# Performance work log

Measured on AMD Instinct MI355X. Metric: run time of the kernel, lower is better.

## Reference

```python
import jax, jax.numpy as jnp
import numpy as np

# static config (matches init_kwargs)
NH, NKV, E, K = 16, 4, 8, 2
CAP_FACTOR = 1.25
LN_EPS = 1e-5


def _layer_norm(x, w, b):
    mu = jnp.mean(x, axis=-1, keepdims=True)
    var = jnp.mean(jnp.square(x - mu), axis=-1, keepdims=True)
    return (x - mu) * jax.lax.rsqrt(var + LN_EPS) * w + b


def setup_inputs() -> dict:
    key = jax.random.key(0)
    ks = jax.random.split(key, 6)
    S, B, H, F = 2048, 1, 1024, 2048
    HD = H // NH
    qkv_out = NKV * ((NH // NKV) + 2) * HD  # 1536
    f32 = jnp.float32
    return {
        "hidden_states": jax.random.normal(ks[0], (S, B, H), f32),
        "ln1_weight": jnp.ones((H,), f32),
        "ln1_bias": jnp.zeros((H,), f32),
        "ln2_weight": jnp.ones((H,), f32),
        "ln2_bias": jnp.zeros((H,), f32),
        "qkv_weight": jax.random.normal(ks[1], (qkv_out, H), f32) * 0.02,
        "proj_weight": jax.random.normal(ks[2], (H, H), f32) * 0.02,
        "router_weight": jax.random.normal(ks[3], (H, E), f32) * 0.02,
        "moe_w1": jax.random.normal(ks[4], (E, H, F), f32) * 0.02,
        "moe_w2": jax.random.normal(ks[5], (F and E, F, H), f32)[:E] * 0.02 if False else jax.random.normal(ks[5], (E, F, H), f32) * 0.02,
    }


def reference(hidden_states, ln1_weight, ln1_bias, ln2_weight, ln2_bias,
              qkv_weight, proj_weight, router_weight, moe_w1, moe_w2):
    S, B, H = hidden_states.shape
    HD = H // NH
    q_per_kv = NH // NKV
    # ---- attention block (cp_size=1: all-to-alls are identity) ----
    ln1 = _layer_norm(hidden_states, ln1_weight, ln1_bias)
    qkv = jnp.einsum('sbh,oh->sbo', ln1, qkv_weight)
    qkv = qkv.reshape(S, B, NKV, (q_per_kv + 2) * HD)
    q = qkv[..., : q_per_kv * HD].reshape(S, B, NH, HD)
    k = qkv[..., q_per_kv * HD:(q_per_kv + 1) * HD]          # [S,B,NKV,HD]
    v = qkv[..., (q_per_kv + 1) * HD:]                        # [S,B,NKV,HD]
    qb = jnp.transpose(q, (1, 2, 0, 3)).reshape(B, NKV, q_per_kv, S, HD)
    kb = jnp.transpose(k, (1, 2, 0, 3))                       # [B,NKV,S,HD]
    vb = jnp.transpose(v, (1, 2, 0, 3))
    scale = 1.0 / np.sqrt(HD).astype(np.float32)
    scores = jnp.einsum('bgqsd,bgtd->bgqst', qb, kb) * scale  # [B,NKV,qpk,S,S]
    causal = jnp.tril(jnp.ones((S, S), bool))
    scores = jnp.where(causal, scores, jnp.finfo(scores.dtype).min)
    attn = jax.nn.softmax(scores, axis=-1)
    ao = jnp.einsum('bgqst,bgtd->bgqsd', attn, vb)
    ao = ao.reshape(B, NH, S, HD)
    ao = jnp.transpose(ao, (2, 0, 1, 3)).reshape(S, B, H)
    proj = jnp.einsum('sbh,oh->sbo', ao, proj_weight)
    h1 = hidden_states + proj
    # ---- MoE block (ep_size=1: uniform all-to-all is identity) ----
    ln2 = _layer_norm(h1, ln2_weight, ln2_bias)
    x = ln2.reshape(-1, H)                                    # [N,H]
    N = x.shape[0]
    logits = x @ router_weight                                # linear(x, router_weight.t())
    probs = jax.nn.softmax(logits, axis=-1)
    top_p, top_i = jax.lax.top_k(probs, K)
    top_p = top_p / jnp.sum(top_p, axis=-1, keepdims=True)
    exp_idx = top_i.reshape(-1)                               # [N*K]
    exp_p = top_p.reshape(-1)
    # stable sort by expert id, capacity-padded dispatch
    order = jnp.argsort(exp_idx, stable=True)
    sorted_exp = exp_idx[order]
    counts = jnp.bincount(exp_idx, length=E)
    offsets = jnp.concatenate([jnp.zeros((1,), counts.dtype), jnp.cumsum(counts)[:-1]])
    within = jnp.arange(N * K) - offsets[sorted_exp]
    cap = int(np.ceil(N * K / E * CAP_FACTOR))
    T = E * cap
    valid = within < cap
    dst = jnp.where(valid, sorted_exp * cap + within, T)      # T = out-of-bounds -> dropped
    padded_tokens = jnp.zeros((T, H), x.dtype).at[dst].set(x[order // K], mode='drop')
    padded_probs = jnp.zeros((T,), exp_p.dtype).at[dst].set(exp_p[order], mode='drop')
    padded_tid = jnp.zeros((T,), jnp.int32).at[dst].set((order // K).astype(jnp.int32), mode='drop')
    # grouped expert GEMMs: [E,cap,H] x [E,H,F] -> gelu -> [E,cap,H]
    xt = padded_tokens.reshape(E, cap, H)
    fc1 = jax.nn.gelu(jnp.einsum('ech,ehf->ecf', xt, moe_w1))
    fc2 = jnp.einsum('ecf,efh->ech', fc1, moe_w2).reshape(T, H)
    weighted = fc2 * padded_probs[:, None]                    # pad slots have prob 0
    moe_out = jnp.zeros((N, H), hidden_states.dtype).at[padded_tid].add(weighted)
    return h1 + moe_out.reshape(S, B, H)
```

## Files before the change

kernel.cpp:

```cpp
#include <hip/hip_runtime.h>
#include <hip/hip_bf16.h>
#include <stdint.h>

#define S_LEN 2048
#define HDIM  1024
#define NHEAD 16
#define NKVH  4
#define HEADD 64
#define QKV_O 1536
#define NEXP  8
#define TOPK  2
#define CAP   640
#define TCAP  (NEXP*CAP)
#define FDIM  2048
#define LOG2E 1.44269504088896f
#define NCHUNK 40

typedef __bf16 bf16x8 __attribute__((ext_vector_type(8)));
typedef float  f32x4  __attribute__((ext_vector_type(4)));
typedef unsigned int u32;
typedef u32 u32x4 __attribute__((ext_vector_type(4)));
typedef u32 u32x2 __attribute__((ext_vector_type(2)));
typedef unsigned short u16;
typedef u16 u16x8 __attribute__((ext_vector_type(8)));

__device__ __forceinline__ void gload16(const __bf16* g, __bf16* l) {
    __builtin_amdgcn_global_load_lds(
        (const __attribute__((address_space(1))) u32*)g,
        (__attribute__((address_space(3))) u32*)l, 16, 0, 0);
}

__device__ __constant__ const signed char c_strip[NCHUNK] =
    {0,1,2,3, 4,4, 5,5, 6,6, 7,7, 8,8,8, 9,9,9, 10,10,10, 11,11,11,
     12,12,12,12, 13,13,13,13, 14,14,14,14, 15,15,15,15};
__device__ __constant__ const signed char c_chunk[NCHUNK] =
    {0,0,0,0, 0,1, 0,1, 0,1, 0,1, 0,1,2, 0,1,2, 0,1,2, 0,1,2,
     0,1,2,3, 0,1,2,3, 0,1,2,3, 0,1,2,3};
__device__ __constant__ const signed char c_cbase[16] = {0,1,2,3,4,6,8,10,12,15,18,21,24,28,32,36};
__device__ __constant__ const signed char c_nch[16]   = {1,1,1,1,2,2,2,2,3,3,3,3,4,4,4,4};

__global__ __launch_bounds__(256)
void prep_kernel(const float* __restrict__ hidden, const float* __restrict__ ln1w,
                 const float* __restrict__ ln1bb, const float* __restrict__ qkvW,
                 const float* __restrict__ projW, __bf16* __restrict__ ln1o,
                 __bf16* __restrict__ qkvWb, __bf16* __restrict__ projWb) {
    const int b = blockIdx.x, tid = threadIdx.x;
    if (b < S_LEN) {
        __shared__ float red[256];
        const float* x = hidden + (size_t)b * HDIM;
        float s = 0.f;
        for (int i = tid; i < HDIM; i += 256) s += x[i];
        red[tid] = s; __syncthreads();
        for (int st = 128; st > 0; st >>= 1) { if (tid < st) red[tid] += red[tid+st]; __syncthreads(); }
        float mu = red[0] / HDIM; __syncthreads();
        float v = 0.f;
        for (int i = tid; i < HDIM; i += 256) { float d = x[i]-mu; v += d*d; }
        red[tid] = v; __syncthreads();
        for (int st = 128; st > 0; st >>= 1) { if (tid < st) red[tid] += red[tid+st]; __syncthreads(); }
        float rstd = rsqrtf(red[0]/HDIM + 1e-5f);
        for (int i = tid; i < HDIM; i += 256)
            ln1o[(size_t)b*HDIM + i] = (__bf16)((x[i]-mu)*rstd*ln1w[i] + ln1bb[i]);
        return;
    }
    const float* src; __bf16* dst; int i;
    if (b < S_LEN + 768) { src = qkvW; dst = qkvWb; i = (b - S_LEN)*256 + tid; }
    else                 { src = projW; dst = projWb; i = (b - S_LEN - 768)*256 + tid; }
    const float4* s = (const float4*)src + (size_t)i*2;
    float4 a = s[0], b4 = s[1];
    __bf16 tmp[8] = {(__bf16)a.x,(__bf16)a.y,(__bf16)a.z,(__bf16)a.w,
                     (__bf16)b4.x,(__bf16)b4.y,(__bf16)b4.z,(__bf16)b4.w};
    *(u32x4*)(dst + (size_t)i*8) = *(u32x4*)tmp;
}

__global__ __launch_bounds__(256)
void transp2_kernel(const float* __restrict__ w1, const float* __restrict__ w2,
                    __bf16* __restrict__ w1t, __bf16* __restrict__ w2t) {
    __shared__ float t[32][33];
    const int b = blockIdx.x;
    const float* src; __bf16* dst; int K, N, n0, k0, e;
    if (b < 16384) {
        e = b >> 11; int rem = b & 2047;
        K = HDIM; N = FDIM; n0 = (rem & 63) * 32; k0 = (rem >> 6) * 32;
        src = w1 + (size_t)e*K*N; dst = w1t + (size_t)e*K*N;
    } else {
        int bb = b - 16384; e = bb >> 11; int rem = bb & 2047;
        K = FDIM; N = HDIM; n0 = (rem & 31) * 32; k0 = (rem >> 5) * 32;
        src = w2 + (size_t)e*K*N; dst = w2t + (size_t)e*K*N;
    }
    int tx = threadIdx.x & 31, ty = threadIdx.x >> 5;
    #pragma unroll
    for (int i = 0; i < 32; i += 8)
        t[ty+i][tx] = src[(size_t)(k0+ty+i)*N + n0 + tx];
    __syncthreads();
    #pragma unroll
    for (int i = 0; i < 32; i += 8)
        dst[(size_t)(n0+ty+i)*K + k0 + tx] = (__bf16)t[tx][ty+i];
}

template<int EPI>
__global__ __launch_bounds__(256)
void gemm_bf16_kernel(const __bf16* __restrict__ A, const __bf16* __restrict__ Bt,
                      const float* __restrict__ R, void* __restrict__ Cout,
                      int N, int K, long sA, long sB, long sC) {
    __shared__ __bf16 As[128*64];
    __shared__ __bf16 Bs[128*64];
    const int e = blockIdx.z;
    A  += (size_t)e * sA;
    Bt += (size_t)e * sB;
    const int m0 = blockIdx.y*128, n0 = blockIdx.x*128;
    const int tid = threadIdx.x;
    const int lane = tid & 63, w = tid >> 6;
    const int lr = lane & 15, lg = lane >> 4;
    const int wr = w >> 1, wc = w & 1;
    const int srow8 = lane >> 3, sg = lane & 7;
    f32x4 acc[4][4] = {};
    for (int k0 = 0; k0 < K; k0 += 64) {
        __syncthreads();
        #pragma unroll
        for (int i = 0; i < 4; ++i) {
            int row = 32*w + 8*i + srow8;
            int src_g = sg ^ (row & 7);
            gload16(A  + (size_t)(m0+row)*K + k0 + src_g*8,
                    (__bf16*)((char*)As + (32*w + 8*i)*128));
            gload16(Bt + (size_t)(n0+row)*K + k0 + src_g*8,
                    (__bf16*)((char*)Bs + (32*w + 8*i)*128));
        }
        __syncthreads();
        #pragma unroll
        for (int ks = 0; ks < 2; ++ks) {
            bf16x8 af[4], bfr[4];
            #pragma unroll
            for (int mi = 0; mi < 4; ++mi) {
                int row = wr*64 + mi*16 + lr;
                af[mi] = *(const bf16x8*)((const char*)As + ((row*128 + (lg+4*ks)*16) ^ ((row&7)<<4)));
            }
            #pragma unroll
            for (int ni = 0; ni < 4; ++ni) {
                int row = wc*64 + ni*16 + lr;
                bfr[ni] = *(const bf16x8*)((const char*)Bs + ((row*128 + (lg+4*ks)*16) ^ ((row&7)<<4)));
            }
            #pragma unroll
            for (int mi = 0; mi < 4; ++mi)
                #pragma unroll
                for (int ni = 0; ni < 4; ++ni)
                    acc[mi][ni] = __builtin_amdgcn_mfma_f32_16x16x32_bf16(af[mi], bfr[ni], acc[mi][ni], 0,0,0);
        }
    }
    #pragma unroll
    for (int mi = 0; mi < 4; ++mi) {
        #pragma unroll
        for (int ni = 0; ni < 4; ++ni) {
            #pragma unroll
            for (int r = 0; r < 4; ++r) {
                int row = m0 + wr*64 + mi*16 + lg*4 + r;
                int col = n0 + wc*64 + ni*16 + lr;
                float v = acc[mi][ni][r];
                if (EPI == 1) v += R[(size_t)row*N + col];
                if (EPI == 2) {
                    float t = 0.7978845608028654f * (v + 0.044715f*v*v*v);
                    v = 0.5f * v * (1.f + tanhf(t));
                }
                if (EPI == 2 || EPI == 3)
                    ((__bf16*)Cout)[(size_t)e*sC + (size_t)row*N + col] = (__bf16)v;
                else
                    ((float*)Cout)[(size_t)e*sC + (size_t)row*N + col] = v;
            }
        }
    }
}

__global__ __launch_bounds__(512)
void attn_part_kernel(const __bf16* __restrict__ qkv, float* __restrict__ partO,
                      float* __restrict__ partML) {
    const int cx = blockIdx.x;
    const int h  = blockIdx.y;
    const int hg = h >> 2, qi = h & 3;
    const int qb = c_strip[cx];
    const int t0 = 4 * c_chunk[cx];
    const int t1 = min(qb + 1, t0 + 4);
    const int q0 = qb * 128;
    const int tid  = threadIdx.x;
    const int w    = tid >> 6;
    const int lane = tid & 63;
    const int lr   = lane & 15;
    const int lg   = lane >> 4;

    __shared__ __attribute__((aligned(16))) __bf16 Kls[128*64];
    __shared__ __attribute__((aligned(16))) __bf16 Vls[64*128];
    __shared__ __attribute__((aligned(16))) __bf16 Pls[8][16*128];

    const int krow = tid >> 2, kc = (tid & 3) * 2;
    const int va = tid & 63,  dg  = tid >> 6;
    u32x4 kreg[2]; u16x8 vreg[2];

    const __bf16* kbase = qkv + hg*384 + 256;
    const __bf16* vbase = qkv + hg*384 + 320;

#define ISSUE(T) do { \
        const __bf16* kp = kbase + (size_t)((T)*128 + krow)*QKV_O + kc*8; \
        kreg[0] = *(const u32x4*)(kp); \
        kreg[1] = *(const u32x4*)(kp + 8); \
        const __bf16* vp = vbase + (size_t)((T)*128 + 2*va)*QKV_O + dg*8; \
        vreg[0] = *(const u16x8*)(vp); \
        vreg[1] = *(const u16x8*)(vp + QKV_O); \
    } while(0)

#define COMMIT() do { \
        char* Kb = (char*)Kls; \
        *(u32x4*)(Kb + ((krow*128 + (kc+0)*16) ^ ((krow&7)<<4))) = kreg[0]; \
        *(u32x4*)(Kb + ((krow*128 + (kc+1)*16) ^ ((krow&7)<<4))) = kreg[1]; \
        char* Vb = (char*)Vls; \
        _Pragma("unroll") \
        for (int j = 0; j < 8; ++j) { \
            int d = dg*8 + j; \
            u32 u = ((u32)vreg[1][j] << 16) | vreg[0][j]; \
            *(u32*)(Vb + ((d*256 + va*4) ^ ((d&7)<<4))) = u; \
        } \
    } while(0)

    const int qrow = q0 + w*16 + lr;
    const __bf16* qp = qkv + (size_t)qrow*QKV_O + hg*384 + qi*64;
    bf16x8 qfrag[2];
    #pragma unroll
    for (int ks = 0; ks < 2; ++ks) {
        bf16x8 qr = *(const bf16x8*)(qp + ks*32 + lg*8);
        #pragma unroll
        for (int j = 0; j < 8; ++j) qfrag[ks][j] = (__bf16)((float)qr[j] * 0.125f);
    }
    bf16x8 ones;
    #pragma unroll
    for (int j = 0; j < 8; ++j) ones[j] = (__bf16)1.0f;

    f32x4 oacc[4] = {};
    f32x4 lcol = {};
    float mrow[4] = {-INFINITY,-INFINITY,-INFINITY,-INFINITY};

    ISSUE(t0);
    for (int t = t0; t < t1; ++t) {
        __syncthreads();
        COMMIT();
        if (t+1 < t1) ISSUE(t+1);
        __syncthreads();

        f32x4 sacc[8] = {};
        const char* Kb = (const char*)Kls;
        #pragma unroll
        for (int f = 0; f < 8; ++f) {
            int row = lr + 16*f;
            int swz = (row & 7) << 4;
            #pragma unroll
            for (int ks = 0; ks < 2; ++ks) {
                bf16x8 kf = *(const bf16x8*)(Kb + ((row*128 + (lg*8+32*ks)*2) ^ swz));
                sacc[f] = __builtin_amdgcn_mfma_f32_16x16x32_bf16(qfrag[ks], kf, sacc[f], 0,0,0);
            }
        }
        if (t == qb) {
            #pragma unroll
            for (int f = 0; f < 8; ++f)
                #pragma unroll
                for (int r = 0; r < 4; ++r)
                    if (lr + 16*f > 16*w + 4*lg + r) sacc[f][r] = -INFINITY;
        }
        float tm[4];
        #pragma unroll
        for (int r = 0; r < 4; ++r) {
            float a = fmaxf(fmaxf(sacc[0][r], sacc[1][r]), fmaxf(sacc[2][r], sacc[3][r]));
            float b2 = fmaxf(fmaxf(sacc[4][r], sacc[5][r]), fmaxf(sacc[6][r], sacc[7][r]));
            tm[r] = fmaxf(a, b2);
        }
        #pragma unroll
        for (int msk = 1; msk < 16; msk <<= 1)
            #pragma unroll
            for (int r = 0; r < 4; ++r) tm[r] = fmaxf(tm[r], __shfl_xor(tm[r], msk, 64));
        float corr[4];
        #pragma unroll
        for (int r = 0; r < 4; ++r) {
            float mn = fmaxf(mrow[r], tm[r]);
            corr[r] = exp2f((mrow[r]-mn)*LOG2E);
            mrow[r] = mn;
        }
        #pragma unroll
        for (int f = 0; f < 8; ++f)
            #pragma unroll
            for (int r = 0; r < 4; ++r)
                sacc[f][r] = exp2f((sacc[f][r]-mrow[r])*LOG2E);
        #pragma unroll
        for (int ct = 0; ct < 4; ++ct)
            #pragma unroll
            for (int r = 0; r < 4; ++r) oacc[ct][r] *= corr[r];
        #pragma unroll
        for (int r = 0; r < 4; ++r) lcol[r] *= corr[r];
        char* Pw = (char*)&Pls[w][0];
        #pragma unroll
        for (int f = 0; f < 8; ++f)
            #pragma unroll
            for (int r = 0; r < 4; ++r) {
                int row = 4*lg + r, col = lr + 16*f;
                *(__bf16*)(Pw + ((row*256 + col*2) ^ ((row&7)<<4))) = (__bf16)sacc[f][r];
            }
        const char* Vb = (const char*)Vls;
        bf16x8 pa[4];
        #pragma unroll
        for (int ks = 0; ks < 4; ++ks)
            pa[ks] = *(const bf16x8*)(Pw + ((lr*256 + (lg*8+32*ks)*2) ^ ((lr&7)<<4)));
        #pragma unroll
        for (int ks = 0; ks < 4; ++ks)
            lcol = __builtin_amdgcn_mfma_f32_16x16x32_bf16(pa[ks], ones, lcol, 0,0,0);
        #pragma unroll
        for (int ct = 0; ct < 4; ++ct) {
            int row = lr + 16*ct;
            int swz = (row & 7) << 4;
            #pragma unroll
            for (int ks = 0; ks < 4; ++ks) {
                bf16x8 vf = *(const bf16x8*)(Vb + ((row*256 + (lg*8+32*ks)*2) ^ swz));
                oacc[ct] = __builtin_amdgcn_mfma_f32_16x16x32_bf16(pa[ks], vf, oacc[ct], 0,0,0);
            }
        }
    }
    const int p = h*NCHUNK + cx;
    float* po = partO + (size_t)p * (128*64);
    #pragma unroll
    for (int ct = 0; ct < 4; ++ct)
        #pragma unroll
        for (int r = 0; r < 4; ++r)
            po[(16*w + 4*lg + r)*64 + 16*ct + lr] = oacc[ct][r];
    if (lr == 0) {
        float* pm = partML + (size_t)p * 256;
        #pragma unroll
        for (int r = 0; r < 4; ++r) {
            pm[(16*w + 4*lg + r)*2    ] = mrow[r];
            pm[(16*w + 4*lg + r)*2 + 1] = lcol[r];
        }
    }
#undef ISSUE
#undef COMMIT
}

__global__ __launch_bounds__(256)
void attn_combine_kernel(const float* __restrict__ partO, const float* __restrict__ partML,
                         __bf16* __restrict__ ao) {
    const int rb = blockIdx.x, h = blockIdx.y;
    const int row0 = rb*8;
    const int qb = row0 >> 7;
    const int nc = c_nch[qb], cb = c_cbase[qb];
    const int tid = threadIdx.x;
    const int rl = tid >> 5, d2 = (tid & 31) * 2;
    const int grow = row0 + rl;
    const int srow = grow & 127;
    const int pbase = h*NCHUNK + cb;
    float mv[4], lv[4];
    float M = -INFINITY;
    for (int c = 0; c < nc; ++c) {
        const float* pm = partML + (size_t)(pbase+c)*256 + srow*2;
        mv[c] = pm[0]; lv[c] = pm[1];
        M = fmaxf(M, mv[c]);
    }
    float L = 0.f, a0 = 0.f, a1 = 0.f;
    for (int c = 0; c < nc; ++c) {
        float wc = exp2f((mv[c]-M)*LOG2E);
        L += wc * lv[c];
        const float* po = partO + (size_t)(pbase+c)*(128*64) + srow*64 + d2;
        a0 += wc * po[0];
        a1 += wc * po[1];
    }
    float inv = 1.f / L;
    __bf16 o2[2] = {(__bf16)(a0*inv), (__bf16)(a1*inv)};
    *(u32*)(ao + (size_t)grow*HDIM + h*64 + d2) = *(u32*)o2;
}

__global__ __launch_bounds__(256)
void ln2_router_kernel(const float* __restrict__ h1, const float* __restrict__ w,
                       const float* __restrict__ b, const float* __restrict__ rw,
                       __bf16* __restrict__ x2b, int* __restrict__ expi,
                       float* __restrict__ expp) {
    const int t = blockIdx.x, tid = threadIdx.x;
    __shared__ float red[256];
    __shared__ float red8[256][8];
    const float* x = h1 + (size_t)t*HDIM;
    float s = 0.f;
    for (int i = tid; i < HDIM; i += 256) s += x[i];
    red[tid] = s; __syncthreads();
    for (int st = 128; st > 0; st >>= 1) { if (tid < st) red[tid] += red[tid+st]; __syncthreads(); }
    float mu = red[0] / HDIM; __syncthreads();
    float v = 0.f;
    for (int i = tid; i < HDIM; i += 256) { float d = x[i]-mu; v += d*d; }
    red[tid] = v; __syncthreads();
    for (int st = 128; st > 0; st >>= 1) { if (tid < st) red[tid] += red[tid+st]; __syncthreads(); }
    float rstd = rsqrtf(red[0]/HDIM + 1e-5f);
    float part[8] = {};
    for (int i = tid; i < HDIM; i += 256) {
        float o = (x[i]-mu)*rstd*w[i] + b[i];
        x2b[(size_t)t*HDIM + i] = (__bf16)o;
        const float* wp = rw + (size_t)i*NEXP;
        #pragma unroll
        for (int e2 = 0; e2 < 8; ++e2) part[e2] += o * wp[e2];
    }
    #pragma unroll
    for (int e2 = 0; e2 < 8; ++e2) red8[tid][e2] = part[e2];
    __syncthreads();
    for (int st = 128; st > 0; st >>= 1) {
        if (tid < st)
            #pragma unroll
            for (int e2 = 0; e2 < 8; ++e2) red8[tid][e2] += red8[tid+st][e2];
        __syncthreads();
    }
    if (tid == 0) {
        float lg[8];
        #pragma unroll
        for (int e2 = 0; e2 < 8; ++e2) lg[e2] = red8[0][e2];
        int i0 = 0;
        for (int e2 = 1; e2 < 8; ++e2) if (lg[e2] > lg[i0]) i0 = e2;
        int i1 = -1;
        for (int e2 = 0; e2 < 8; ++e2) { if (e2 == i0) continue; if (i1 < 0 || lg[e2] > lg[i1]) i1 = e2; }
        float p1 = __expf(lg[i1] - lg[i0]);
        float inv = 1.f / (1.f + p1);
        expi[t*2]   = i0; expi[t*2+1] = i1;
        expp[t*2]   = inv; expp[t*2+1] = p1 * inv;
    }
}

__global__ __launch_bounds__(256)
void dst_fast_kernel(const int* __restrict__ expi, int* __restrict__ dst) {
    __shared__ int hist[256][9];
    const int tid = threadIdx.x;
    int ev[16];
    #pragma unroll
    for (int i = 0; i < 16; i += 4)
        *(int4*)(ev+i) = *(const int4*)(expi + tid*16 + i);
    int cnt[8] = {};
    #pragma unroll
    for (int i = 0; i < 16; ++i)
        #pragma unroll
        for (int e = 0; e < 8; ++e) cnt[e] += (ev[i] == e);
    #pragma unroll
    for (int e = 0; e < 8; ++e) hist[tid][e] = cnt[e];
    __syncthreads();
    const int w = tid >> 6, lane = tid & 63;
    #pragma unroll
    for (int rep = 0; rep < 2; ++rep) {
        int e = w + rep*4;
        int h0 = hist[4*lane+0][e], h1 = hist[4*lane+1][e],
            h2 = hist[4*lane+2][e], h3 = hist[4*lane+3][e];
        int s = h0+h1+h2+h3, inc = s;
        #pragma unroll
        for (int off = 1; off < 64; off <<= 1) {
            int v = __shfl_up(inc, off, 64);
            if (lane >= off) inc += v;
        }
        int excl = inc - s;
        hist[4*lane+0][e] = excl;
        hist[4*lane+1][e] = excl + h0;
        hist[4*lane+2][e] = excl + h0 + h1;
        hist[4*lane+3][e] = excl + h0 + h1 + h2;
    }
    __syncthreads();
    int run[8];
    #pragma unroll
    for (int e = 0; e < 8; ++e) run[e] = hist[tid][e];
    int out[16];
    #pragma unroll
    for (int i = 0; i < 16; ++i) {
        int e = ev[i], within = 0;
        #pragma unroll
        for (int e2 = 0; e2 < 8; ++e2)
            if (e == e2) { within = run[e2]; run[e2]++; }
        out[i] = (within < CAP) ? (e*CAP + within) : -1;
    }
    #pragma unroll
    for (int i = 0; i < 16; i += 4)
        *(int4*)(dst + tid*16 + i) = *(const int4*)(out+i);
}

__global__ void scatter_kernel(const __bf16* __restrict__ x2b, const int* __restrict__ dst,
                               __bf16* __restrict__ xt) {
    int s = blockIdx.x;
    int d = dst[s];
    if (d < 0) return;
    int t = s >> 1;
    int i = threadIdx.x;
    u32x2 v = *(const u32x2*)(x2b + (size_t)t*HDIM + i*4);
    *(u32x2*)(xt + (size_t)d*HDIM + i*4) = v;
}

__global__ void combine_kernel(const float* __restrict__ h1, const float* __restrict__ fc2,
                               const int* __restrict__ dst, const float* __restrict__ expp,
                               float* __restrict__ out) {
    int t = blockIdx.x;
    int d0 = dst[t*2], d1 = dst[t*2+1];
    float p0 = expp[t*2], p1 = expp[t*2+1];
    for (int i = threadIdx.x; i < HDIM; i += 256) {
        float v = h1[(size_t)t*HDIM + i];
        if (d0 >= 0) v += p0 * fc2[(size_t)d0*HDIM + i];
        if (d1 >= 0) v += p1 * fc2[(size_t)d1*HDIM + i];
        out[(size_t)t*HDIM + i] = v;
    }
}

extern "C" void kernel_launch(void* const* d_in, const int* in_sizes, int n_in,
                              void* d_out, int out_size, void* d_ws, size_t ws_size,
                              hipStream_t stream) {
    const float* hidden = (const float*)d_in[0];
    const float* ln1w   = (const float*)d_in[1];
    const float* ln1b_  = (const float*)d_in[2];
    const float* ln2w   = (const float*)d_in[3];
    const float* ln2b_  = (const float*)d_in[4];
    const float* qkvW   = (const float*)d_in[5];
    const float* projW  = (const float*)d_in[6];
    const float* routW  = (const float*)d_in[7];
    const float* w1     = (const float*)d_in[8];
    const float* w2     = (const float*)d_in[9];
    float* out = (float*)d_out;

    char* base = (char*)d_ws;
    __bf16* w1t    = (__bf16*)(base);
    __bf16* w2t    = (__bf16*)(base + 33554432);
    __bf16* ln1b   = (__bf16*)(base + 0);
    __bf16* qkvWb  = (__bf16*)(base + 4194304);
    __bf16* qkvb   = (__bf16*)(base + 7340032);
    __bf16* aob    = (__bf16*)(base + 13631488);
    __bf16* projWb = (__bf16*)(base + 17825792);
    char* B0 = base + 67108864;
    float*  h1   = (float*)(B0);
    __bf16* xtb  = (__bf16*)(B0 + 8388608);
    __bf16* fc1b = (__bf16*)(B0 + 18874368);
    float*  fc2  = (float*)(B0 + 39845888);
    __bf16* x2b  = (__bf16*)fc2;
    int*    expi = (int*)(B0 + 60817408);
    int*    dsts = (int*)(B0 + 60833792);
    float*  expp = (float*)(B0 + 60850176);
    float*  partML = (float*)xtb;
    float*  partO  = (float*)fc1b;

    prep_kernel<<<S_LEN + 768 + 512, 256, 0, stream>>>(
        hidden, ln1w, ln1b_, qkvW, projW, ln1b, qkvWb, projWb);
    gemm_bf16_kernel<3><<<dim3(QKV_O/128, S_LEN/128, 1), 256, 0, stream>>>(
        ln1b, qkvWb, nullptr, qkvb, QKV_O, HDIM, 0, 0, 0);
    attn_part_kernel<<<dim3(NCHUNK, NHEAD), 512, 0, stream>>>(qkvb, partO, partML);
    attn_combine_kernel<<<dim3(S_LEN/8, NHEAD), 256, 0, stream>>>(partO, partML, aob);
    gemm_bf16_kernel<1><<<dim3(HDIM/128, S_LEN/128, 1), 256, 0, stream>>>(
        aob, projWb, hidden, h1, HDIM, HDIM, 0, 0, 0);
    ln2_router_kernel<<<S_LEN, 256, 0, stream>>>(h1, ln2w, ln2b_, routW, x2b, expi, expp);
    dst_fast_kernel<<<1, 256, 0, stream>>>(expi, dsts);
    scatter_kernel<<<S_LEN*TOPK, 256, 0, stream>>>(x2b, dsts, xtb);
    transp2_kernel<<<32768, 256, 0, stream>>>(w1, w2, w1t, w2t);
    gemm_bf16_kernel<2><<<dim3(FDIM/128, CAP/128, NEXP), 256, 0, stream>>>(
        xtb, w1t, nullptr, fc1b, FDIM, HDIM,
        (long)CAP*HDIM, (long)FDIM*HDIM, (long)CAP*FDIM);
    gemm_bf16_kernel<0><<<dim3(HDIM/128, CAP/128, NEXP), 256, 0, stream>>>(
        fc1b, w2t, nullptr, fc2, HDIM, FDIM,
        (long)CAP*FDIM, (long)FDIM*HDIM, (long)CAP*HDIM);
    combine_kernel<<<S_LEN, 256, 0, stream>>>(h1, fc2, dsts, expp, out);
}
```

Measured before the change: 255.7 us.

## Vectorize weight transpose, cache rows in LayerNorm, vectorize MoE combine

The expert-weight transpose kernel now uses 64x64 tiles, reading rows with float4 loads and writing 16-byte bf16 stores, so it launches a quarter as many blocks. Both LayerNorm kernels keep each thread's four elements in registers instead of reloading them from global memory for every pass. The MoE combine kernel switches to float4 loads and stores. The prep_kernel parameter order is also swapped to match the swapped call arguments, which leaves behaviour unchanged. The transpose of the 128 MB of fp32 expert weights is probably the main cost these changes target, and the larger LDS tile may lower occupancy.

```diff
diff --git a/kernel.cpp b/kernel.cpp
--- a/kernel.cpp
+++ b/kernel.cpp
@@ -43,23 +43,29 @@
 void prep_kernel(const float* __restrict__ hidden, const float* __restrict__ ln1w,
                  const float* __restrict__ ln1bb, const float* __restrict__ qkvW,
                  const float* __restrict__ projW, __bf16* __restrict__ ln1o,
-                 __bf16* __restrict__ qkvWb, __bf16* __restrict__ projWb) {
+                 __bf16* __restrict__ projWb, __bf16* __restrict__ qkvWb) {
     const int b = blockIdx.x, tid = threadIdx.x;
     if (b < S_LEN) {
         __shared__ float red[256];
         const float* x = hidden + (size_t)b * HDIM;
-        float s = 0.f;
-        for (int i = tid; i < HDIM; i += 256) s += x[i];
+        float xr[4];
+        #pragma unroll
+        for (int j = 0; j < 4; ++j) xr[j] = x[tid + 256*j];
+        float s = xr[0] + xr[1] + xr[2] + xr[3];
         red[tid] = s; __syncthreads();
         for (int st = 128; st > 0; st >>= 1) { if (tid < st) red[tid] += red[tid+st]; __syncthreads(); }
         float mu = red[0] / HDIM; __syncthreads();
         float v = 0.f;
-        for (int i = tid; i < HDIM; i += 256) { float d = x[i]-mu; v += d*d; }
+        #pragma unroll
+        for (int j = 0; j < 4; ++j) { float d = xr[j]-mu; v += d*d; }
         red[tid] = v; __syncthreads();
         for (int st = 128; st > 0; st >>= 1) { if (tid < st) red[tid] += red[tid+st]; __syncthreads(); }
         float rstd = rsqrtf(red[0]/HDIM + 1e-5f);
-        for (int i = tid; i < HDIM; i += 256)
-            ln1o[(size_t)b*HDIM + i] = (__bf16)((x[i]-mu)*rstd*ln1w[i] + ln1bb[i]);
+        #pragma unroll
+        for (int j = 0; j < 4; ++j) {
+            int i = tid + 256*j;
+            ln1o[(size_t)b*HDIM + i] = (__bf16)((xr[j]-mu)*rstd*ln1w[i] + ln1bb[i]);
+        }
         return;
     }
     const float* src; __bf16* dst; int i;
@@ -75,26 +81,36 @@
 __global__ __launch_bounds__(256)
 void transp2_kernel(const float* __restrict__ w1, const float* __restrict__ w2,
                     __bf16* __restrict__ w1t, __bf16* __restrict__ w2t) {
-    __shared__ float t[32][33];
+    __shared__ float t[64][65];
     const int b = blockIdx.x;
-    const float* src; __bf16* dst; int K, N, n0, k0, e;
-    if (b < 16384) {
-        e = b >> 11; int rem = b & 2047;
-        K = HDIM; N = FDIM; n0 = (rem & 63) * 32; k0 = (rem >> 6) * 32;
+    const float* src; __bf16* dst; int K, N, n0, k0;
+    if (b < 4096) {
+        int e = b >> 9, rem = b & 511;
+        K = HDIM; N = FDIM; n0 = (rem & 31) * 64; k0 = (rem >> 5) * 64;
         src = w1 + (size_t)e*K*N; dst = w1t + (size_t)e*K*N;
     } else {
-        int bb = b - 16384; e = bb >> 11; int rem = bb & 2047;
-        K = FDIM; N = HDIM; n0 = (rem & 31) * 32; k0 = (rem >> 5) * 32;
+        int bb = b - 4096; int e = bb >> 9, rem = bb & 511;
+        K = FDIM; N = HDIM; n0 = (rem & 15) * 64; k0 = (rem >> 4) * 64;
         src = w2 + (size_t)e*K*N; dst = w2t + (size_t)e*K*N;
     }
-    int tx = threadIdx.x & 31, ty = threadIdx.x >> 5;
-    #pragma unroll
-    for (int i = 0; i < 32; i += 8)
-        t[ty+i][tx] = src[(size_t)(k0+ty+i)*N + n0 + tx];
+    const int tid = threadIdx.x;
+    const int r = tid >> 4, c4 = (tid & 15) * 4;
+    #pragma unroll
+    for (int i = 0; i < 4; ++i) {
+        float4 v = *(const float4*)(src + (size_t)(k0 + r + 16*i)*N + n0 + c4);
+        t[r+16*i][c4+0] = v.x; t[r+16*i][c4+1] = v.y;
+        t[r+16*i][c4+2] = v.z; t[r+16*i][c4+3] = v.w;
+    }
     __syncthreads();
-    #pragma unroll
-    for (int i = 0; i < 32; i += 8)
-        dst[(size_t)(n0+ty+i)*K + k0 + tx] = (__bf16)t[tx][ty+i];
+    const int rn = tid >> 3, kc = (tid & 7) * 8;
+    #pragma unroll
+    for (int i = 0; i < 2; ++i) {
+        int n = rn + 32*i;
+        __bf16 tmp[8];
+        #pragma unroll
+        for (int j = 0; j < 8; ++j) tmp[j] = (__bf16)t[kc+j][n];
+        *(u32x4*)(dst + (size_t)(n0+n)*K + k0 + kc) = *(u32x4*)tmp;
+    }
 }
 
 template<int EPI>
@@ -377,19 +393,24 @@
     __shared__ float red[256];
     __shared__ float red8[256][8];
     const float* x = h1 + (size_t)t*HDIM;
-    float s = 0.f;
-    for (int i = tid; i < HDIM; i += 256) s += x[i];
+    float xr[4];
+    #pragma unroll
+    for (int j = 0; j < 4; ++j) xr[j] = x[tid + 256*j];
+    float s = xr[0] + xr[1] + xr[2] + xr[3];
     red[tid] = s; __syncthreads();
     for (int st = 128; st > 0; st >>= 1) { if (tid < st) red[tid] += red[tid+st]; __syncthreads(); }
     float mu = red[0] / HDIM; __syncthreads();
     float v = 0.f;
-    for (int i = tid; i < HDIM; i += 256) { float d = x[i]-mu; v += d*d; }
+    #pragma unroll
+    for (int j = 0; j < 4; ++j) { float d = xr[j]-mu; v += d*d; }
     red[tid] = v; __syncthreads();
     for (int st = 128; st > 0; st >>= 1) { if (tid < st) red[tid] += red[tid+st]; __syncthreads(); }
     float rstd = rsqrtf(red[0]/HDIM + 1e-5f);
     float part[8] = {};
-    for (int i = tid; i < HDIM; i += 256) {
-        float o = (x[i]-mu)*rstd*w[i] + b[i];
+    #pragma unroll
+    for (int j = 0; j < 4; ++j) {
+        int i = tid + 256*j;
+        float o = (xr[j]-mu)*rstd*w[i] + b[i];
         x2b[(size_t)t*HDIM + i] = (__bf16)o;
         const float* wp = rw + (size_t)i*NEXP;
         #pragma unroll
@@ -488,12 +509,17 @@
     int t = blockIdx.x;
     int d0 = dst[t*2], d1 = dst[t*2+1];
     float p0 = expp[t*2], p1 = expp[t*2+1];
-    for (int i = threadIdx.x; i < HDIM; i += 256) {
-        float v = h1[(size_t)t*HDIM + i];
-        if (d0 >= 0) v += p0 * fc2[(size_t)d0*HDIM + i];
-        if (d1 >= 0) v += p1 * fc2[(size_t)d1*HDIM + i];
-        out[(size_t)t*HDIM + i] = v;
-    }
+    int i = threadIdx.x * 4;
+    float4 v = *(const float4*)(h1 + (size_t)t*HDIM + i);
+    if (d0 >= 0) {
+        float4 f = *(const float4*)(fc2 + (size_t)d0*HDIM + i);
+        v.x += p0*f.x; v.y += p0*f.y; v.z += p0*f.z; v.w += p0*f.w;
+    }
+    if (d1 >= 0) {
+        float4 f = *(const float4*)(fc2 + (size_t)d1*HDIM + i);
+        v.x += p1*f.x; v.y += p1*f.y; v.z += p1*f.z; v.w += p1*f.w;
+    }
+    *(float4*)(out + (size_t)t*HDIM + i) = v;
 }
 
 extern "C" void kernel_launch(void* const* d_in, const int* in_sizes, int n_in,
@@ -532,7 +558,7 @@
     float*  partO  = (float*)fc1b;
 
     prep_kernel<<<S_LEN + 768 + 512, 256, 0, stream>>>(
-        hidden, ln1w, ln1b_, qkvW, projW, ln1b, qkvWb, projWb);
+        hidden, ln1w, ln1b_, qkvW, projW, ln1b, projWb, qkvWb);
     gemm_bf16_kernel<3><<<dim3(QKV_O/128, S_LEN/128, 1), 256, 0, stream>>>(
         ln1b, qkvWb, nullptr, qkvb, QKV_O, HDIM, 0, 0, 0);
     attn_part_kernel<<<dim3(NCHUNK, NHEAD), 512, 0, stream>>>(qkvb, partO, partML);
@@ -542,7 +568,7 @@
     ln2_router_kernel<<<S_LEN, 256, 0, stream>>>(h1, ln2w, ln2b_, routW, x2b, expi, expp);
     dst_fast_kernel<<<1, 256, 0, stream>>>(expi, dsts);
     scatter_kernel<<<S_LEN*TOPK, 256, 0, stream>>>(x2b, dsts, xtb);
-    transp2_kernel<<<32768, 256, 0, stream>>>(w1, w2, w1t, w2t);
+    transp2_kernel<<<8192, 256, 0, stream>>>(w1, w2, w1t, w2t);
     gemm_bf16_kernel<2><<<dim3(FDIM/128, CAP/128, NEXP), 256, 0, stream>>>(
         xtb, w1t, nullptr, fc1b, FDIM, HDIM,
         (long)CAP*HDIM, (long)FDIM*HDIM, (long)CAP*FDIM);
```

Result: faster. 250.2 us (-2.2%).
